# Kernel tuning notes

Measured on AMD Instinct MI355X. Metric: run time of the kernel, lower is better.

## Reference

```python
import jax, jax.numpy as jnp
import numpy as np

N, E, D, H, L = 10000, 80000, 1024, 8, 2
C = D // H          # 128 per-head channels
NEG = 0.2           # GATv2 default negative_slope


def setup_inputs() -> dict:
    k = jax.random.split(jax.random.key(0), 16)
    s = 0.02
    return {
        "x": jax.random.normal(k[0], (N, D), jnp.float32),
        "edge_index": jax.random.randint(k[1], (2, E), 0, N),
        "edge_attr": jax.random.randint(k[2], (E,), 0, 3),
        "node_types": jax.random.randint(k[3], (N,), 0, 5),
        "node_type_emb": s * jax.random.normal(k[4], (5, D), jnp.float32),
        "edge_type_emb": s * jax.random.normal(k[5], (3, D), jnp.float32),
        "Wl": s * jax.random.normal(k[6], (L, D, D), jnp.float32),
        "bl": jnp.zeros((L, D), jnp.float32),
        "Wr": s * jax.random.normal(k[7], (L, D, D), jnp.float32),
        "br": jnp.zeros((L, D), jnp.float32),
        "We": s * jax.random.normal(k[8], (L, D, D), jnp.float32),
        "att": s * jax.random.normal(k[9], (L, H, C), jnp.float32),
        "conv_bias": jnp.zeros((L, D), jnp.float32),
        "out_W": s * jax.random.normal(k[10], (D, D), jnp.float32),
        "out_b": jnp.zeros((D,), jnp.float32),
    }


def _gatv2(h, src, dst, ee, Wl, bl, Wr, br, We, att, b):
    """PyG GATv2Conv: concat=True, add_self_loops=True (fill_value='mean')."""
    n = h.shape[0]
    xl = (h @ Wl + bl).reshape(n, H, C)   # source transform (lin_l)
    xr = (h @ Wr + br).reshape(n, H, C)   # target transform (lin_r)
    # self loops: edge_attr of a loop = mean of raw incoming edge feats
    cnt = jax.ops.segment_sum(jnp.ones(src.shape, jnp.float32), dst, num_segments=n)
    loop_attr = jax.ops.segment_sum(ee, dst, num_segments=n) / jnp.maximum(cnt, 1.0)[:, None]
    loops = jnp.arange(n)
    s2 = jnp.concatenate([src, loops])
    d2 = jnp.concatenate([dst, loops])
    ea = jnp.concatenate([ee, loop_attr], axis=0)          # [E+N, D]
    ep = (ea @ We).reshape(-1, H, C)                        # lin_edge (no bias)
    e = jax.nn.leaky_relu(xl[s2] + xr[d2] + ep, NEG)        # [E+N, H, C]
    logit = jnp.einsum('ehc,hc->eh', e, att)                # attention logits
    # segment softmax over destination nodes (every node has a self loop)
    m = jax.ops.segment_max(logit, d2, num_segments=n)
    a = jnp.exp(logit - m[d2])
    alpha = a / jax.ops.segment_sum(a, d2, num_segments=n)[d2]
    out = jax.ops.segment_sum(alpha[:, :, None] * xl[s2], d2, num_segments=n)
    return out.reshape(n, D) + b


def reference(x, edge_index, edge_attr, node_types, node_type_emb, edge_type_emb,
              Wl, bl, Wr, br, We, att, conv_bias, out_W, out_b):
    h = x + node_type_emb[node_types]
    ee = edge_type_emb[edge_attr]
    src, dst = edge_index[0], edge_index[1]
    for i in range(L):  # num_layers = 2
        h = h + jax.nn.relu(_gatv2(h, src, dst, ee, Wl[i], bl[i], Wr[i], br[i],
                                   We[i], att[i], conv_bias[i]))
    return h @ out_W + out_b
```

## Files before the change

kernel.cpp:

```cpp
#include <hip/hip_runtime.h>
#include <hip/hip_bf16.h>
#include <stdint.h>

typedef __bf16 bf16_t;
typedef bf16_t bf16x8 __attribute__((ext_vector_type(8)));
typedef bf16_t bf16x4 __attribute__((ext_vector_type(4)));
typedef float f32x4 __attribute__((ext_vector_type(4)));

#define NN 10000
#define EE 80000
#define DD 1024
#define LL 2
#define MPAD 10112
#define NEGS 0.2f

#define GLOAD_LDS16(g, l) \
    __builtin_amdgcn_global_load_lds((__attribute__((address_space(1))) void*)(void*)(g), \
                                     (__attribute__((address_space(3))) void*)(l), 16, 0, 0)

__global__ __launch_bounds__(256)
void transpose_batch(const float* __restrict__ Wl, const float* __restrict__ Wr,
                     const float* __restrict__ outW,
                     bf16_t* __restrict__ WT, bf16_t* __restrict__ OWT)
{
    __shared__ float tile[32][33];
    int z = blockIdx.z;
    const float* src;
    bf16_t* dstp;
    switch (z) {
        case 0: src = Wl;                       dstp = WT;                           break;
        case 1: src = Wr;                       dstp = WT + (size_t)1024*1024;       break;
        case 2: src = Wl + (size_t)1024*1024;   dstp = WT + (size_t)2*1024*1024;     break;
        case 3: src = Wr + (size_t)1024*1024;   dstp = WT + (size_t)3*1024*1024;     break;
        default: src = outW;                    dstp = OWT;                          break;
    }
    int bx = blockIdx.x, by = blockIdx.y;
    int tx = threadIdx.x & 31, ty = threadIdx.x >> 5;
#pragma unroll
    for (int i = 0; i < 4; ++i)
        tile[ty + i*8][tx] = src[(size_t)(by*32 + ty + i*8)*1024 + bx*32 + tx];
    __syncthreads();
#pragma unroll
    for (int i = 0; i < 4; ++i)
        dstp[(size_t)(bx*32 + ty + i*8)*1024 + by*32 + tx] = (bf16_t)tile[tx][ty + i*8];
}

__global__ __launch_bounds__(256)
void h_init(const float* __restrict__ x, const int* __restrict__ ntypes,
            const float* __restrict__ nte, bf16_t* __restrict__ hbuf)
{
    size_t idx = ((size_t)blockIdx.x*256 + threadIdx.x) * 8;
    if (idx >= (size_t)MPAD*1024) return;
    int n = (int)(idx >> 10);
    int c = (int)(idx & 1023);
    bf16x8 outv;
    if (n < NN) {
        const float* xp = x + (size_t)n*1024 + c;
        int t = ntypes[n];
        const float* ep = nte + (size_t)t*1024 + c;
#pragma unroll
        for (int j = 0; j < 8; ++j) outv[j] = (bf16_t)(xp[j] + ep[j]);
    } else {
#pragma unroll
        for (int j = 0; j < 8; ++j) outv[j] = (bf16_t)0.f;
    }
    *(bf16x8*)(hbuf + idx) = outv;
}

__global__ void zero_i32(int* p, int n)
{ int i = blockIdx.x*256 + threadIdx.x; if (i < n) p[i] = 0; }

__global__ void zero_f32(float* p, int n)
{ int i = blockIdx.x*256 + threadIdx.x; if (i < n) p[i] = 0.f; }

__global__ void hist_k(const int* __restrict__ dsts, int* __restrict__ deg)
{ int e = blockIdx.x*256 + threadIdx.x; if (e < EE) atomicAdd(&deg[dsts[e]], 1); }

__global__ void scan_block(const int* __restrict__ deg, int* __restrict__ inc,
                           int* __restrict__ bsums)
{
    __shared__ int sdata[256];
    int i = blockIdx.x*256 + threadIdx.x;
    int v = (i < NN) ? deg[i] : 0;
    sdata[threadIdx.x] = v;
    __syncthreads();
    for (int d = 1; d < 256; d <<= 1) {
        int t = (threadIdx.x >= d) ? sdata[threadIdx.x - d] : 0;
        __syncthreads();
        sdata[threadIdx.x] += t;
        __syncthreads();
    }
    if (i < NN) inc[i] = sdata[threadIdx.x];
    if (threadIdx.x == 255) bsums[blockIdx.x] = sdata[255];
}

__global__ void scan_sums(int* bsums, int nb)
{
    if (threadIdx.x == 0 && blockIdx.x == 0) {
        int run = 0;
        for (int i = 0; i < nb; ++i) { int v = bsums[i]; bsums[i] = run; run += v; }
    }
}

__global__ void finalize_rp(const int* __restrict__ inc, const int* __restrict__ bsums,
                            int* __restrict__ rp)
{
    int i = blockIdx.x*256 + threadIdx.x;
    if (i < NN) rp[i+1] = inc[i] + bsums[i >> 8];
    if (i == 0) rp[0] = 0;
}

__global__ void copy_i32(const int* __restrict__ a, int* __restrict__ b, int n)
{ int i = blockIdx.x*256 + threadIdx.x; if (i < n) b[i] = a[i]; }

__global__ void fill_csr(const int* __restrict__ srcs, const int* __restrict__ dsts,
                         const int* __restrict__ etype, int* __restrict__ cursor,
                         int* __restrict__ sorted_src, int* __restrict__ sorted_typ)
{
    int e = blockIdx.x*256 + threadIdx.x;
    if (e < EE) {
        int d = dsts[e];
        int pos = atomicAdd(&cursor[d], 1);
        sorted_src[pos] = srcs[e];
        sorted_typ[pos] = etype[e];
    }
}

__global__ void pack_all_bias(const float* __restrict__ bl, const float* __restrict__ br,
                              const float* __restrict__ outb, float* __restrict__ biasb)
{
    int i = blockIdx.x*256 + threadIdx.x;
    if (i < 4096) {
        int l = i >> 11, j = i & 2047;
        biasb[i] = (j < 1024) ? bl[l*1024 + j] : br[l*1024 + j - 1024];
    } else if (i < 5120) {
        biasb[i] = outb[i - 4096];
    }
}

__global__ __launch_bounds__(256)
void compute_m3(const float* __restrict__ ete, const float* __restrict__ WeL,
                float* __restrict__ M3)
{
    int j  = (blockIdx.x & 3) * 256 + threadIdx.x;
    int k0 = (blockIdx.x >> 2) * 16;
    float a0 = 0.f, a1 = 0.f, a2 = 0.f;
#pragma unroll
    for (int kk = 0; kk < 16; ++kk) {
        int k = k0 + kk;
        float w = WeL[(size_t)k*1024 + j];
        a0 += ete[k]        * w;
        a1 += ete[1024 + k] * w;
        a2 += ete[2048 + k] * w;
    }
    atomicAdd(&M3[j],        a0);
    atomicAdd(&M3[1024 + j], a1);
    atomicAdd(&M3[2048 + j], a2);
}

template <typename OT>
__global__ __launch_bounds__(256)
void gemm_bt(const bf16_t* __restrict__ A, const bf16_t* __restrict__ BT,
             const float* __restrict__ bias, OT* __restrict__ Cmat,
             int K, int Ntot, int storeM, int mtiles, int ntiles)
{
    __shared__ __align__(16) bf16_t As[128*64];
    __shared__ __align__(16) bf16_t Bs[128*64];
    const int tid  = threadIdx.x;
    const int wave = tid >> 6;
    const int lane = tid & 63;

    const int GROUP_M = 8;
    int pid = blockIdx.x;
    int in_group = GROUP_M * ntiles;
    int gid = pid / in_group;
    int first_m = gid * GROUP_M;
    int gsz = mtiles - first_m; if (gsz > GROUP_M) gsz = GROUP_M;
    int local = pid % in_group;
    const int m0 = (first_m + (local % gsz)) * 128;
    const int n0 = (local / gsz) * 128;

    const int wm = (wave & 1) * 64;
    const int wn = (wave >> 1) * 64;
    const int quad = lane >> 4;
    const int l16  = lane & 15;

    const int srow = lane >> 3;
    const int gcol = ((lane & 7) ^ srow) * 8;

    f32x4 acc[4][4];
    f32x4 zero = {0.f, 0.f, 0.f, 0.f};
#pragma unroll
    for (int i = 0; i < 4; ++i)
#pragma unroll
        for (int j = 0; j < 4; ++j) acc[i][j] = zero;

    const bf16_t* aBase = A  + (size_t)(m0 + wave*8 + srow) * K + gcol;
    const bf16_t* bBase = BT + (size_t)(n0 + wave*8 + srow) * K + gcol;
    bf16_t* asDst = As + wave*512;
    bf16_t* bsDst = Bs + wave*512;

    for (int k0 = 0; k0 < K; k0 += 64) {
#pragma unroll
        for (int j = 0; j < 4; ++j)
            GLOAD_LDS16(aBase + (size_t)(j*32)*K + k0, asDst + j*2048);
#pragma unroll
        for (int j = 0; j < 4; ++j)
            GLOAD_LDS16(bBase + (size_t)(j*32)*K + k0, bsDst + j*2048);
        __syncthreads();
#pragma unroll
        for (int kk = 0; kk < 2; ++kk) {
            bf16x8 af[4], bfr[4];
#pragma unroll
            for (int mi = 0; mi < 4; ++mi) {
                int row = wm + mi*16 + l16;
                int ch  = ((kk*4 + quad) ^ (row & 7)) * 8;
                af[mi] = *(const bf16x8*)(As + row*64 + ch);
            }
#pragma unroll
            for (int ni = 0; ni < 4; ++ni) {
                int row = wn + ni*16 + l16;
                int ch  = ((kk*4 + quad) ^ (row & 7)) * 8;
                bfr[ni] = *(const bf16x8*)(Bs + row*64 + ch);
            }
#pragma unroll
            for (int mi = 0; mi < 4; ++mi)
#pragma unroll
                for (int ni = 0; ni < 4; ++ni)
                    acc[mi][ni] = __builtin_amdgcn_mfma_f32_16x16x32_bf16(af[mi], bfr[ni], acc[mi][ni], 0, 0, 0);
        }
        __syncthreads();
    }

#pragma unroll
    for (int mi = 0; mi < 4; ++mi) {
#pragma unroll
        for (int ni = 0; ni < 4; ++ni) {
            int col = n0 + wn + ni*16 + l16;
            float bv = bias[col];
#pragma unroll
            for (int r = 0; r < 4; ++r) {
                int row = m0 + wm + mi*16 + quad*4 + r;
                if (row < storeM)
                    Cmat[(size_t)row * Ntot + col] = (OT)(acc[mi][ni][r] + bv);
            }
        }
    }
}

__global__ __launch_bounds__(256)
void fused_edge(const int* __restrict__ rp, const int* __restrict__ ssrc,
                const int* __restrict__ styp, const bf16_t* __restrict__ XLXR,
                const float* __restrict__ M3, const float* __restrict__ attv,
                const float* __restrict__ cbias, bf16_t* __restrict__ hbuf)
{
    int node = blockIdx.x;
    int tid = threadIdx.x;
    int c = tid * 4;
    __shared__ int s_src[256];
    __shared__ int s_typ[256];

    int b = rp[node], en = rp[node + 1];

    bf16x4 xlv = *(const bf16x4*)(XLXR + (size_t)node*2048 + c);
    bf16x4 xrv = *(const bf16x4*)(XLXR + (size_t)node*2048 + 1024 + c);
    float xr0 = (float)xrv[0], xr1 = (float)xrv[1], xr2 = (float)xrv[2], xr3 = (float)xrv[3];
    float at0 = attv[c], at1 = attv[c+1], at2 = attv[c+2], at3 = attv[c+3];
    float m3r[3][4];
#pragma unroll
    for (int t = 0; t < 3; ++t)
#pragma unroll
        for (int j = 0; j < 4; ++j) m3r[t][j] = M3[t*1024 + c + j];

    float a0 = 0.f, a1 = 0.f, a2 = 0.f, a3 = 0.f;
    float den = 0.f;
    float cnt0 = 0.f, cnt1 = 0.f, cnt2 = 0.f;

    for (int base = b; base < en; base += 256) {
        int nchunk = en - base; if (nchunk > 256) nchunk = 256;
        __syncthreads();
        if (tid < nchunk) { s_src[tid] = ssrc[base + tid]; s_typ[tid] = styp[base + tid]; }
        __syncthreads();
        for (int i = 0; i < nchunk; ++i) {
            int s = s_src[i];
            int t = s_typ[i];
            bf16x4 xs = *(const bf16x4*)(XLXR + (size_t)s*2048 + c);
            float x0 = (float)xs[0], x1 = (float)xs[1], x2 = (float)xs[2], x3 = (float)xs[3];
            float v0 = x0 + xr0 + m3r[t][0]; v0 = (v0 > 0.f) ? v0 : NEGS * v0;
            float v1 = x1 + xr1 + m3r[t][1]; v1 = (v1 > 0.f) ? v1 : NEGS * v1;
            float v2 = x2 + xr2 + m3r[t][2]; v2 = (v2 > 0.f) ? v2 : NEGS * v2;
            float v3 = x3 + xr3 + m3r[t][3]; v3 = (v3 > 0.f) ? v3 : NEGS * v3;
            float part = v0*at0 + v1*at1 + v2*at2 + v3*at3;
            part += __shfl_xor(part, 1);
            part += __shfl_xor(part, 2);
            part += __shfl_xor(part, 4);
            part += __shfl_xor(part, 8);
            part += __shfl_xor(part, 16);
            part = fminf(fmaxf(part, -60.f), 60.f);
            float p = __expf(part);
            cnt0 += (t == 0) ? 1.f : 0.f;
            cnt1 += (t == 1) ? 1.f : 0.f;
            cnt2 += (t == 2) ? 1.f : 0.f;
            den += p;
            a0 += p * x0; a1 += p * x1; a2 += p * x2; a3 += p * x3;
        }
    }

    float deg = cnt0 + cnt1 + cnt2;
    float inv = 1.f / fmaxf(deg, 1.f);
    float w0 = cnt0 * inv, w1 = cnt1 * inv, w2 = cnt2 * inv;
    float sx0 = (float)xlv[0], sx1 = (float)xlv[1], sx2 = (float)xlv[2], sx3 = (float)xlv[3];
    float e0 = w0*m3r[0][0] + w1*m3r[1][0] + w2*m3r[2][0];
    float e1 = w0*m3r[0][1] + w1*m3r[1][1] + w2*m3r[2][1];
    float e2 = w0*m3r[0][2] + w1*m3r[1][2] + w2*m3r[2][2];
    float e3 = w0*m3r[0][3] + w1*m3r[1][3] + w2*m3r[2][3];
    float u0 = sx0 + xr0 + e0; u0 = (u0 > 0.f) ? u0 : NEGS * u0;
    float u1 = sx1 + xr1 + e1; u1 = (u1 > 0.f) ? u1 : NEGS * u1;
    float u2 = sx2 + xr2 + e2; u2 = (u2 > 0.f) ? u2 : NEGS * u2;
    float u3 = sx3 + xr3 + e3; u3 = (u3 > 0.f) ? u3 : NEGS * u3;
    float sp = u0*at0 + u1*at1 + u2*at2 + u3*at3;
    sp += __shfl_xor(sp, 1);
    sp += __shfl_xor(sp, 2);
    sp += __shfl_xor(sp, 4);
    sp += __shfl_xor(sp, 8);
    sp += __shfl_xor(sp, 16);
    sp = fminf(fmaxf(sp, -60.f), 60.f);
    float ps = __expf(sp);
    den += ps;
    a0 += ps * sx0; a1 += ps * sx1; a2 += ps * sx2; a3 += ps * sx3;

    float invd = 1.f / den;
    bf16x4 hv = *(const bf16x4*)(hbuf + (size_t)node*1024 + c);
    const float* cb = cbias + c;
    bf16x4 outv;
    outv[0] = (bf16_t)((float)hv[0] + fmaxf(a0*invd + cb[0], 0.f));
    outv[1] = (bf16_t)((float)hv[1] + fmaxf(a1*invd + cb[1], 0.f));
    outv[2] = (bf16_t)((float)hv[2] + fmaxf(a2*invd + cb[2], 0.f));
    outv[3] = (bf16_t)((float)hv[3] + fmaxf(a3*invd + cb[3], 0.f));
    *(bf16x4*)(hbuf + (size_t)node*1024 + c) = outv;
}

extern "C" void kernel_launch(void* const* d_in, const int* in_sizes, int n_in,
                              void* d_out, int out_size, void* d_ws, size_t ws_size,
                              hipStream_t stream)
{
    (void)in_sizes; (void)n_in; (void)out_size; (void)ws_size;
    const float* x     = (const float*)d_in[0];
    const int*   eidx  = (const int*)d_in[1];
    const int*   etype = (const int*)d_in[2];
    const int*   ntyp  = (const int*)d_in[3];
    const float* nte   = (const float*)d_in[4];
    const float* ete   = (const float*)d_in[5];
    const float* Wl    = (const float*)d_in[6];
    const float* bl    = (const float*)d_in[7];
    const float* Wr    = (const float*)d_in[8];
    const float* br    = (const float*)d_in[9];
    const float* We    = (const float*)d_in[10];
    const float* attw  = (const float*)d_in[11];
    const float* cbias = (const float*)d_in[12];
    const float* outW  = (const float*)d_in[13];
    const float* outb  = (const float*)d_in[14];
    const int* srcs = eidx;
    const int* dsts = eidx + EE;

    char* wsp = (char*)d_ws;
    size_t off = 0;
    auto carve = [&](size_t bytes) -> void* {
        void* pp = wsp + off;
        off += (bytes + 255) & ~(size_t)255;
        return pp;
    };
    bf16_t* hbuf  = (bf16_t*)carve((size_t)MPAD*1024*2);
    bf16_t* XLXR  = (bf16_t*)carve((size_t)MPAD*2048*2);
    bf16_t* WT    = (bf16_t*)carve((size_t)LL*2048*1024*2);
    bf16_t* OWT   = (bf16_t*)carve((size_t)1024*1024*2);
    float*  M3L   = (float*)carve((size_t)LL*3072*4);
    float*  biasb = (float*)carve(5120*4);
    int* deg    = (int*)carve((size_t)NN*4);
    int* rp     = (int*)carve((size_t)(NN+1)*4);
    int* cursor = (int*)carve((size_t)NN*4);
    int* ssrc   = (int*)carve((size_t)EE*4);
    int* styp   = (int*)carve((size_t)EE*4);
    int* incb   = (int*)carve((size_t)NN*4);
    int* bsums  = (int*)carve(64*4);

    transpose_batch<<<dim3(32, 32, 5), 256, 0, stream>>>(Wl, Wr, outW, WT, OWT);
    h_init<<<5056, 256, 0, stream>>>(x, ntyp, nte, hbuf);
    pack_all_bias<<<20, 256, 0, stream>>>(bl, br, outb, biasb);

    zero_f32<<<(LL*3072 + 255)/256, 256, 0, stream>>>(M3L, LL*3072);
    for (int l = 0; l < LL; ++l)
        compute_m3<<<256, 256, 0, stream>>>(ete, We + (size_t)l*1024*1024, M3L + l*3072);

    zero_i32<<<40, 256, 0, stream>>>(deg, NN);
    hist_k<<<(EE + 255)/256, 256, 0, stream>>>(dsts, deg);
    scan_block<<<40, 256, 0, stream>>>(deg, incb, bsums);
    scan_sums<<<1, 64, 0, stream>>>(bsums, 40);
    finalize_rp<<<40, 256, 0, stream>>>(incb, bsums, rp);
    copy_i32<<<40, 256, 0, stream>>>(rp, cursor, NN);
    fill_csr<<<(EE + 255)/256, 256, 0, stream>>>(srcs, dsts, etype, cursor, ssrc, styp);

    for (int l = 0; l < LL; ++l) {
        gemm_bt<bf16_t><<<79*16, 256, 0, stream>>>(hbuf, WT + (size_t)l*2048*1024,
                                                   biasb + l*2048, XLXR,
                                                   1024, 2048, MPAD, 79, 16);
        fused_edge<<<NN, 256, 0, stream>>>(rp, ssrc, styp, XLXR, M3L + l*3072, attw + l*1024,
                                           cbias + l*1024, hbuf);
    }

    gemm_bt<float><<<79*8, 256, 0, stream>>>(hbuf, OWT, biasb + 4096, (float*)d_out,
                                             1024, 1024, NN, 79, 8);
}
```

Measured before the change: 417.9 us.

## Merge preamble kernels, single-block CSR scan, and wave-parallel edge attention

Combines the weight transpose, h init, bias packing and buffer zeroing into one launch, and merges the two per-layer M3 launches and the four scan kernels into single launches to cut launch count. The edge kernel now computes logits with one wave per edge (16 channels per lane), staging M3 in shared memory and exp values in a shared buffer. A second pass then does the weighted aggregation. This trades extra barriers, shared memory and LDS atomics for fewer serial per-edge reductions across 256 threads.

```diff
diff --git a/kernel.cpp b/kernel.cpp
--- a/kernel.cpp
+++ b/kernel.cpp
@@ -19,99 +19,134 @@
                                      (__attribute__((address_space(3))) void*)(l), 16, 0, 0)
 
 __global__ __launch_bounds__(256)
-void transpose_batch(const float* __restrict__ Wl, const float* __restrict__ Wr,
-                     const float* __restrict__ outW,
-                     bf16_t* __restrict__ WT, bf16_t* __restrict__ OWT)
+void preamble(const float* __restrict__ Wl, const float* __restrict__ Wr,
+              const float* __restrict__ outW, bf16_t* __restrict__ WT,
+              bf16_t* __restrict__ OWT,
+              const float* __restrict__ x, const int* __restrict__ ntypes,
+              const float* __restrict__ nte, bf16_t* __restrict__ hbuf,
+              const float* __restrict__ bl, const float* __restrict__ br,
+              const float* __restrict__ outb, float* __restrict__ biasb,
+              float* __restrict__ M3L, int* __restrict__ deg)
 {
     __shared__ float tile[32][33];
-    int z = blockIdx.z;
-    const float* src;
-    bf16_t* dstp;
-    switch (z) {
-        case 0: src = Wl;                       dstp = WT;                           break;
-        case 1: src = Wr;                       dstp = WT + (size_t)1024*1024;       break;
-        case 2: src = Wl + (size_t)1024*1024;   dstp = WT + (size_t)2*1024*1024;     break;
-        case 3: src = Wr + (size_t)1024*1024;   dstp = WT + (size_t)3*1024*1024;     break;
-        default: src = outW;                    dstp = OWT;                          break;
-    }
-    int bx = blockIdx.x, by = blockIdx.y;
-    int tx = threadIdx.x & 31, ty = threadIdx.x >> 5;
-#pragma unroll
-    for (int i = 0; i < 4; ++i)
-        tile[ty + i*8][tx] = src[(size_t)(by*32 + ty + i*8)*1024 + bx*32 + tx];
-    __syncthreads();
-#pragma unroll
-    for (int i = 0; i < 4; ++i)
-        dstp[(size_t)(bx*32 + ty + i*8)*1024 + by*32 + tx] = (bf16_t)tile[tx][ty + i*8];
+    int b = blockIdx.x;
+    int tid = threadIdx.x;
+    if (b < 5120) {
+        int z = b >> 10, rem = b & 1023;
+        int bx = rem & 31, by = rem >> 5;
+        const float* src;
+        bf16_t* dstp;
+        switch (z) {
+            case 0: src = Wl;                       dstp = WT;                        break;
+            case 1: src = Wr;                       dstp = WT + (size_t)1024*1024;    break;
+            case 2: src = Wl + (size_t)1024*1024;   dstp = WT + (size_t)2*1024*1024;  break;
+            case 3: src = Wr + (size_t)1024*1024;   dstp = WT + (size_t)3*1024*1024;  break;
+            default: src = outW;                    dstp = OWT;                       break;
+        }
+        int tx = tid & 31, ty = tid >> 5;
+#pragma unroll
+        for (int i = 0; i < 4; ++i)
+            tile[ty + i*8][tx] = src[(size_t)(by*32 + ty + i*8)*1024 + bx*32 + tx];
+        __syncthreads();
+#pragma unroll
+        for (int i = 0; i < 4; ++i)
+            dstp[(size_t)(bx*32 + ty + i*8)*1024 + by*32 + tx] = (bf16_t)tile[tx][ty + i*8];
+    } else if (b < 10176) {
+        size_t idx = ((size_t)(b - 5120)*256 + tid) * 8;
+        if (idx >= (size_t)MPAD*1024) return;
+        int n = (int)(idx >> 10);
+        int c = (int)(idx & 1023);
+        bf16x8 outv;
+        if (n < NN) {
+            const float* xp = x + (size_t)n*1024 + c;
+            int t = ntypes[n];
+            const float* ep = nte + (size_t)t*1024 + c;
+#pragma unroll
+            for (int j = 0; j < 8; ++j) outv[j] = (bf16_t)(xp[j] + ep[j]);
+        } else {
+#pragma unroll
+            for (int j = 0; j < 8; ++j) outv[j] = (bf16_t)0.f;
+        }
+        *(bf16x8*)(hbuf + idx) = outv;
+    } else if (b < 10196) {
+        int i = (b - 10176)*256 + tid;
+        if (i < 4096) {
+            int l = i >> 11, j = i & 2047;
+            biasb[i] = (j < 1024) ? bl[l*1024 + j] : br[l*1024 + j - 1024];
+        } else if (i < 5120) {
+            biasb[i] = outb[i - 4096];
+        }
+    } else if (b < 10220) {
+        int i = (b - 10196)*256 + tid;
+        if (i < LL*3072) M3L[i] = 0.f;
+    } else {
+        int i = (b - 10220)*256 + tid;
+        if (i < NN) deg[i] = 0;
+    }
 }
 
 __global__ __launch_bounds__(256)
-void h_init(const float* __restrict__ x, const int* __restrict__ ntypes,
-            const float* __restrict__ nte, bf16_t* __restrict__ hbuf)
-{
-    size_t idx = ((size_t)blockIdx.x*256 + threadIdx.x) * 8;
-    if (idx >= (size_t)MPAD*1024) return;
-    int n = (int)(idx >> 10);
-    int c = (int)(idx & 1023);
-    bf16x8 outv;
-    if (n < NN) {
-        const float* xp = x + (size_t)n*1024 + c;
-        int t = ntypes[n];
-        const float* ep = nte + (size_t)t*1024 + c;
-#pragma unroll
-        for (int j = 0; j < 8; ++j) outv[j] = (bf16_t)(xp[j] + ep[j]);
-    } else {
-#pragma unroll
-        for (int j = 0; j < 8; ++j) outv[j] = (bf16_t)0.f;
-    }
-    *(bf16x8*)(hbuf + idx) = outv;
-}
-
-__global__ void zero_i32(int* p, int n)
-{ int i = blockIdx.x*256 + threadIdx.x; if (i < n) p[i] = 0; }
-
-__global__ void zero_f32(float* p, int n)
-{ int i = blockIdx.x*256 + threadIdx.x; if (i < n) p[i] = 0.f; }
+void compute_m3_all(const float* __restrict__ ete, const float* __restrict__ We,
+                    float* __restrict__ M3L)
+{
+    int l   = blockIdx.x >> 8;
+    int bid = blockIdx.x & 255;
+    const float* WeL = We + (size_t)l*1024*1024;
+    float* M3 = M3L + l*3072;
+    int j  = (bid & 3) * 256 + threadIdx.x;
+    int k0 = (bid >> 2) * 16;
+    float a0 = 0.f, a1 = 0.f, a2 = 0.f;
+#pragma unroll
+    for (int kk = 0; kk < 16; ++kk) {
+        int k = k0 + kk;
+        float w = WeL[(size_t)k*1024 + j];
+        a0 += ete[k]        * w;
+        a1 += ete[1024 + k] * w;
+        a2 += ete[2048 + k] * w;
+    }
+    atomicAdd(&M3[j],        a0);
+    atomicAdd(&M3[1024 + j], a1);
+    atomicAdd(&M3[2048 + j], a2);
+}
 
 __global__ void hist_k(const int* __restrict__ dsts, int* __restrict__ deg)
 { int e = blockIdx.x*256 + threadIdx.x; if (e < EE) atomicAdd(&deg[dsts[e]], 1); }
 
-__global__ void scan_block(const int* __restrict__ deg, int* __restrict__ inc,
-                           int* __restrict__ bsums)
-{
-    __shared__ int sdata[256];
-    int i = blockIdx.x*256 + threadIdx.x;
-    int v = (i < NN) ? deg[i] : 0;
-    sdata[threadIdx.x] = v;
+__global__ __launch_bounds__(1024)
+void scan_csr(const int* __restrict__ deg, int* __restrict__ rp, int* __restrict__ cursor)
+{
+    __shared__ int tot[1024];
+    int t = threadIdx.x;
+    int base = t * 10;
+    int v[10];
+    int run = 0;
+#pragma unroll
+    for (int j = 0; j < 10; ++j) {
+        int i = base + j;
+        int d = (i < NN) ? deg[i] : 0;
+        run += d;
+        v[j] = run;
+    }
+    tot[t] = run;
     __syncthreads();
-    for (int d = 1; d < 256; d <<= 1) {
-        int t = (threadIdx.x >= d) ? sdata[threadIdx.x - d] : 0;
-        __syncthreads();
-        sdata[threadIdx.x] += t;
-        __syncthreads();
-    }
-    if (i < NN) inc[i] = sdata[threadIdx.x];
-    if (threadIdx.x == 255) bsums[blockIdx.x] = sdata[255];
-}
-
-__global__ void scan_sums(int* bsums, int nb)
-{
-    if (threadIdx.x == 0 && blockIdx.x == 0) {
-        int run = 0;
-        for (int i = 0; i < nb; ++i) { int v = bsums[i]; bsums[i] = run; run += v; }
-    }
-}
-
-__global__ void finalize_rp(const int* __restrict__ inc, const int* __restrict__ bsums,
-                            int* __restrict__ rp)
-{
-    int i = blockIdx.x*256 + threadIdx.x;
-    if (i < NN) rp[i+1] = inc[i] + bsums[i >> 8];
-    if (i == 0) rp[0] = 0;
-}
-
-__global__ void copy_i32(const int* __restrict__ a, int* __restrict__ b, int n)
-{ int i = blockIdx.x*256 + threadIdx.x; if (i < n) b[i] = a[i]; }
+    for (int d = 1; d < 1024; d <<= 1) {
+        int xv = (t >= d) ? tot[t - d] : 0;
+        __syncthreads();
+        tot[t] += xv;
+        __syncthreads();
+    }
+    int ex = (t == 0) ? 0 : tot[t - 1];
+#pragma unroll
+    for (int j = 0; j < 10; ++j) {
+        int i = base + j;
+        if (i < NN) {
+            int incl = ex + v[j];
+            rp[i + 1] = incl;
+            if (i + 1 < NN) cursor[i + 1] = incl;
+        }
+    }
+    if (t == 0) { rp[0] = 0; cursor[0] = 0; }
+}
 
 __global__ void fill_csr(const int* __restrict__ srcs, const int* __restrict__ dsts,
                          const int* __restrict__ etype, int* __restrict__ cursor,
@@ -124,38 +159,6 @@
         sorted_src[pos] = srcs[e];
         sorted_typ[pos] = etype[e];
     }
-}
-
-__global__ void pack_all_bias(const float* __restrict__ bl, const float* __restrict__ br,
-                              const float* __restrict__ outb, float* __restrict__ biasb)
-{
-    int i = blockIdx.x*256 + threadIdx.x;
-    if (i < 4096) {
-        int l = i >> 11, j = i & 2047;
-        biasb[i] = (j < 1024) ? bl[l*1024 + j] : br[l*1024 + j - 1024];
-    } else if (i < 5120) {
-        biasb[i] = outb[i - 4096];
-    }
-}
-
-__global__ __launch_bounds__(256)
-void compute_m3(const float* __restrict__ ete, const float* __restrict__ WeL,
-                float* __restrict__ M3)
-{
-    int j  = (blockIdx.x & 3) * 256 + threadIdx.x;
-    int k0 = (blockIdx.x >> 2) * 16;
-    float a0 = 0.f, a1 = 0.f, a2 = 0.f;
-#pragma unroll
-    for (int kk = 0; kk < 16; ++kk) {
-        int k = k0 + kk;
-        float w = WeL[(size_t)k*1024 + j];
-        a0 += ete[k]        * w;
-        a1 += ete[1024 + k] * w;
-        a2 += ete[2048 + k] * w;
-    }
-    atomicAdd(&M3[j],        a0);
-    atomicAdd(&M3[1024 + j], a1);
-    atomicAdd(&M3[2048 + j], a2);
 }
 
 template <typename OT>
@@ -254,66 +257,95 @@
                 const float* __restrict__ M3, const float* __restrict__ attv,
                 const float* __restrict__ cbias, bf16_t* __restrict__ hbuf)
 {
+    __shared__ float s_m3[3072];
+    __shared__ float s_p[256*8];
+    __shared__ int s_src[256];
+    __shared__ int s_typ[256];
+    __shared__ int s_cnt[3];
+
     int node = blockIdx.x;
     int tid = threadIdx.x;
+    int lane = tid & 63;
+    int wave = tid >> 6;
+
+    for (int i = tid; i < 3072; i += 256) s_m3[i] = M3[i];
+    if (tid < 3) s_cnt[tid] = 0;
+
+    int b = rp[node], en = rp[node + 1];
+
+    int c16 = lane * 16;
+    bf16x8 xra = *(const bf16x8*)(XLXR + (size_t)node*2048 + 1024 + c16);
+    bf16x8 xrb = *(const bf16x8*)(XLXR + (size_t)node*2048 + 1024 + c16 + 8);
+    float xr16[16], at16[16];
+#pragma unroll
+    for (int j = 0; j < 8; ++j) { xr16[j] = (float)xra[j]; xr16[8+j] = (float)xrb[j]; }
+#pragma unroll
+    for (int j = 0; j < 16; ++j) at16[j] = attv[c16 + j];
+
     int c = tid * 4;
-    __shared__ int s_src[256];
-    __shared__ int s_typ[256];
-
-    int b = rp[node], en = rp[node + 1];
-
+    int head = tid >> 5;
     bf16x4 xlv = *(const bf16x4*)(XLXR + (size_t)node*2048 + c);
     bf16x4 xrv = *(const bf16x4*)(XLXR + (size_t)node*2048 + 1024 + c);
-    float xr0 = (float)xrv[0], xr1 = (float)xrv[1], xr2 = (float)xrv[2], xr3 = (float)xrv[3];
     float at0 = attv[c], at1 = attv[c+1], at2 = attv[c+2], at3 = attv[c+3];
-    float m3r[3][4];
-#pragma unroll
-    for (int t = 0; t < 3; ++t)
-#pragma unroll
-        for (int j = 0; j < 4; ++j) m3r[t][j] = M3[t*1024 + c + j];
 
     float a0 = 0.f, a1 = 0.f, a2 = 0.f, a3 = 0.f;
     float den = 0.f;
-    float cnt0 = 0.f, cnt1 = 0.f, cnt2 = 0.f;
 
     for (int base = b; base < en; base += 256) {
         int nchunk = en - base; if (nchunk > 256) nchunk = 256;
         __syncthreads();
         if (tid < nchunk) { s_src[tid] = ssrc[base + tid]; s_typ[tid] = styp[base + tid]; }
         __syncthreads();
-        for (int i = 0; i < nchunk; ++i) {
+        for (int i = wave; i < nchunk; i += 4) {
             int s = s_src[i];
             int t = s_typ[i];
-            bf16x4 xs = *(const bf16x4*)(XLXR + (size_t)s*2048 + c);
-            float x0 = (float)xs[0], x1 = (float)xs[1], x2 = (float)xs[2], x3 = (float)xs[3];
-            float v0 = x0 + xr0 + m3r[t][0]; v0 = (v0 > 0.f) ? v0 : NEGS * v0;
-            float v1 = x1 + xr1 + m3r[t][1]; v1 = (v1 > 0.f) ? v1 : NEGS * v1;
-            float v2 = x2 + xr2 + m3r[t][2]; v2 = (v2 > 0.f) ? v2 : NEGS * v2;
-            float v3 = x3 + xr3 + m3r[t][3]; v3 = (v3 > 0.f) ? v3 : NEGS * v3;
-            float part = v0*at0 + v1*at1 + v2*at2 + v3*at3;
+            bf16x8 xa = *(const bf16x8*)(XLXR + (size_t)s*2048 + c16);
+            bf16x8 xb = *(const bf16x8*)(XLXR + (size_t)s*2048 + c16 + 8);
+            const float* m3p = s_m3 + t*1024 + c16;
+            float part = 0.f;
+#pragma unroll
+            for (int j = 0; j < 8; ++j) {
+                float v = (float)xa[j] + xr16[j] + m3p[j];
+                v = (v > 0.f) ? v : NEGS * v;
+                part += v * at16[j];
+            }
+#pragma unroll
+            for (int j = 0; j < 8; ++j) {
+                float v = (float)xb[j] + xr16[8+j] + m3p[8+j];
+                v = (v > 0.f) ? v : NEGS * v;
+                part += v * at16[8+j];
+            }
             part += __shfl_xor(part, 1);
             part += __shfl_xor(part, 2);
             part += __shfl_xor(part, 4);
-            part += __shfl_xor(part, 8);
-            part += __shfl_xor(part, 16);
-            part = fminf(fmaxf(part, -60.f), 60.f);
-            float p = __expf(part);
-            cnt0 += (t == 0) ? 1.f : 0.f;
-            cnt1 += (t == 1) ? 1.f : 0.f;
-            cnt2 += (t == 2) ? 1.f : 0.f;
+            if ((lane & 7) == 0) {
+                part = fminf(fmaxf(part, -60.f), 60.f);
+                s_p[i*8 + (lane >> 3)] = __expf(part);
+            }
+            if (lane == 0) atomicAdd(&s_cnt[t], 1);
+        }
+        __syncthreads();
+#pragma unroll 2
+        for (int i = 0; i < nchunk; ++i) {
+            float p = s_p[i*8 + head];
+            bf16x4 xs = *(const bf16x4*)(XLXR + (size_t)s_src[i]*2048 + c);
             den += p;
-            a0 += p * x0; a1 += p * x1; a2 += p * x2; a3 += p * x3;
-        }
-    }
-
-    float deg = cnt0 + cnt1 + cnt2;
-    float inv = 1.f / fmaxf(deg, 1.f);
+            a0 += p*(float)xs[0]; a1 += p*(float)xs[1];
+            a2 += p*(float)xs[2]; a3 += p*(float)xs[3];
+        }
+    }
+    __syncthreads();
+
+    float cnt0 = (float)s_cnt[0], cnt1 = (float)s_cnt[1], cnt2 = (float)s_cnt[2];
+    float degf = cnt0 + cnt1 + cnt2;
+    float inv = 1.f / fmaxf(degf, 1.f);
     float w0 = cnt0 * inv, w1 = cnt1 * inv, w2 = cnt2 * inv;
     float sx0 = (float)xlv[0], sx1 = (float)xlv[1], sx2 = (float)xlv[2], sx3 = (float)xlv[3];
-    float e0 = w0*m3r[0][0] + w1*m3r[1][0] + w2*m3r[2][0];
-    float e1 = w0*m3r[0][1] + w1*m3r[1][1] + w2*m3r[2][1];
-    float e2 = w0*m3r[0][2] + w1*m3r[1][2] + w2*m3r[2][2];
-    float e3 = w0*m3r[0][3] + w1*m3r[1][3] + w2*m3r[2][3];
+    float xr0 = (float)xrv[0], xr1 = (float)xrv[1], xr2 = (float)xrv[2], xr3 = (float)xrv[3];
+    float e0 = w0*s_m3[c+0] + w1*s_m3[1024+c+0] + w2*s_m3[2048+c+0];
+    float e1 = w0*s_m3[c+1] + w1*s_m3[1024+c+1] + w2*s_m3[2048+c+1];
+    float e2 = w0*s_m3[c+2] + w1*s_m3[1024+c+2] + w2*s_m3[2048+c+2];
+    float e3 = w0*s_m3[c+3] + w1*s_m3[1024+c+3] + w2*s_m3[2048+c+3];
     float u0 = sx0 + xr0 + e0; u0 = (u0 > 0.f) ? u0 : NEGS * u0;
     float u1 = sx1 + xr1 + e1; u1 = (u1 > 0.f) ? u1 : NEGS * u1;
     float u2 = sx2 + xr2 + e2; u2 = (u2 > 0.f) ? u2 : NEGS * u2;
@@ -381,23 +413,13 @@
     int* cursor = (int*)carve((size_t)NN*4);
     int* ssrc   = (int*)carve((size_t)EE*4);
     int* styp   = (int*)carve((size_t)EE*4);
-    int* incb   = (int*)carve((size_t)NN*4);
-    int* bsums  = (int*)carve(64*4);
-
-    transpose_batch<<<dim3(32, 32, 5), 256, 0, stream>>>(Wl, Wr, outW, WT, OWT);
-    h_init<<<5056, 256, 0, stream>>>(x, ntyp, nte, hbuf);
-    pack_all_bias<<<20, 256, 0, stream>>>(bl, br, outb, biasb);
-
-    zero_f32<<<(LL*3072 + 255)/256, 256, 0, stream>>>(M3L, LL*3072);
-    for (int l = 0; l < LL; ++l)
-        compute_m3<<<256, 256, 0, stream>>>(ete, We + (size_t)l*1024*1024, M3L + l*3072);
-
-    zero_i32<<<40, 256, 0, stream>>>(deg, NN);
+
+    preamble<<<10260, 256, 0, stream>>>(Wl, Wr, outW, WT, OWT,
+                                        x, ntyp, nte, hbuf,
+                                        bl, br, outb, biasb, M3L, deg);
+    compute_m3_all<<<512, 256, 0, stream>>>(ete, We, M3L);
     hist_k<<<(EE + 255)/256, 256, 0, stream>>>(dsts, deg);
-    scan_block<<<40, 256, 0, stream>>>(deg, incb, bsums);
-    scan_sums<<<1, 64, 0, stream>>>(bsums, 40);
-    finalize_rp<<<40, 256, 0, stream>>>(incb, bsums, rp);
-    copy_i32<<<40, 256, 0, stream>>>(rp, cursor, NN);
+    scan_csr<<<1, 1024, 0, stream>>>(deg, rp, cursor);
     fill_csr<<<(EE + 255)/256, 256, 0, stream>>>(srcs, dsts, etype, cursor, ssrc, styp);
 
     for (int l = 0; l < LL; ++l) {
```

Result: slower. 475.7 us (+13.8%).
